# Performance work log

Measured on AMD Instinct MI355X. Metric: run time of the kernel, lower is better.

The kernel has to match this reference:

```python
import jax, jax.numpy as jnp
import numpy as np

TOPK = 16  # module init arg
EPS = 1e-12  # F.normalize eps


def setup_inputs() -> dict:
    key = jax.random.key(0)
    k1, k2, k3 = jax.random.split(key, 3)
    b, c, h, w = 2, 256, 96, 96
    rc = max(c // 4, 16)  # reduced_channels = 64
    x = jax.random.normal(k1, (b, c, h, w), dtype=jnp.float32)
    # 1x1 convs are channel-mixing matmuls; store weights as [out_ch, in_ch]
    w_reduce = jax.random.normal(k2, (rc, c), dtype=jnp.float32) * 0.05
    w_proj = jax.random.normal(k3, (c, rc), dtype=jnp.float32) * 0.05
    return {"x": x, "w_reduce": w_reduce, "w_proj": w_proj}


def reference(x, w_reduce, w_proj):
    b, c, h, w = x.shape
    n = h * w
    # reduce: 1x1 conv == channel matmul -> [b, rc, N]
    feat = jnp.einsum('rc,bchw->brhw', w_reduce, x).reshape(b, -1, n)
    # F.normalize(dim=1): divide by max(L2-norm over channels, eps)
    nrm = jnp.maximum(jnp.sqrt(jnp.sum(feat * feat, axis=1, keepdims=True)), EPS)
    nf = jnp.transpose(feat / nrm, (0, 2, 1))  # [b, N, rc]
    # cosine similarity matrix [b, N, N]
    sim = jnp.einsum('bnr,bmr->bnm', nf, nf)
    k = min(TOPK, n)
    _, idx = jax.lax.top_k(sim, k)  # [b, N, k]
    # gather top-k neighbor features and average -> [b, N, rc]
    corr = jax.vmap(lambda f, i: f[i].mean(axis=1))(nf, idx)
    # proj: 1x1 conv back to C channels, NCHW layout
    enhanced = jnp.einsum('cr,bnr->bnc', w_proj, corr)
    enhanced = jnp.transpose(enhanced, (0, 2, 1)).reshape(b, c, h, w)
    return x + enhanced
```

## Files before the change

### kernel.cpp

```cpp
#include <hip/hip_runtime.h>
#include <cstdint>
#include <cstddef>

#define NPIX 9216
#define NB 2
#define NC 256
#define RC 64
#define TK 16
#define NROWS (NB * NPIX)
#define CT 128
#define NQ 24
#define ECOLS 384
#define NTE 3
#define MAXC 128
#define LCAP 32
#define MARGIN 0.008f

typedef unsigned short ushort_t;
typedef unsigned int uint_t;
typedef __bf16 bf16x8 __attribute__((ext_vector_type(8)));
typedef float f32x4 __attribute__((ext_vector_type(4)));

__device__ __forceinline__ uint_t f2bf(float x) {
  uint_t u = __float_as_uint(x);
  return (u + 0x7FFFu + ((u >> 16) & 1u)) >> 16;
}

__device__ __forceinline__ uint_t ordu(float v) {
  uint_t u = __float_as_uint(v);
  return (u & 0x80000000u) ? ~u : (u | 0x80000000u);
}

#define GL2LDS(gsrc, ldst)                                                   \
  __builtin_amdgcn_global_load_lds(                                          \
      (const __attribute__((address_space(1))) uint_t*)(const void*)(gsrc),  \
      (__attribute__((address_space(3))) uint_t*)(void*)(ldst), 16, 0, 0)

__device__ __forceinline__ void stage_tile(
    const ushort_t* __restrict__ gtile, ushort_t* shbuf, int tid) {
  const int wave = tid >> 6, l = tid & 63;
  const int lr = l >> 3;
  const int ls = (l & 7) ^ lr;
  const ushort_t* g = gtile + (size_t)lr * 64 + ls * 8;
#pragma unroll
  for (int i = 0; i < 4; ++i) {
    const int j = wave * 4 + i;
    GL2LDS(g + (size_t)j * 512, shbuf + j * 512);
  }
}

__global__ __launch_bounds__(256) void k_reduce_norm(
    const float* __restrict__ x, const float* __restrict__ wr,
    float* __restrict__ nf, ushort_t* __restrict__ hi) {
  __shared__ float wl[NC * RC];
  const int tid = threadIdx.x;

  {
    float4 tmp[16];
    const float* wcol = wr + tid;
#pragma unroll
    for (int j = 0; j < 16; ++j) {
      tmp[j].x = wcol[(size_t)(4 * j + 0) * NC];
      tmp[j].y = wcol[(size_t)(4 * j + 1) * NC];
      tmp[j].z = wcol[(size_t)(4 * j + 2) * NC];
      tmp[j].w = wcol[(size_t)(4 * j + 3) * NC];
    }
    float4* wrow = (float4*)(wl + (size_t)tid * RC);
#pragma unroll
    for (int j = 0; j < 16; ++j) wrow[j] = tmp[j];
  }

  const int pl = tid >> 2, rq = tid & 3;
  const int row = blockIdx.x * 64 + pl;
  const int b = row >= NPIX;
  const int n = row - b * NPIX;
  const float* xp = x + (size_t)b * NC * NPIX + n;
  __syncthreads();

  float s[16];
#pragma unroll
  for (int i = 0; i < 16; ++i) s[i] = 0.f;

#pragma unroll 1
  for (int half = 0; half < 4; ++half) {
    float p4[16];
#pragma unroll
    for (int i = 0; i < 16; ++i) p4[i] = 0.f;
#pragma unroll 8
    for (int cl = 0; cl < 64; ++cl) {
      const int c = half * 64 + cl;
      const float xv = xp[(size_t)c * NPIX];
      const float4* w4 = (const float4*)(wl + c * RC + rq * 16);
#pragma unroll
      for (int i = 0; i < 4; ++i) {
        float4 w = w4[i];
        p4[i * 4 + 0] += w.x * xv; p4[i * 4 + 1] += w.y * xv;
        p4[i * 4 + 2] += w.z * xv; p4[i * 4 + 3] += w.w * xv;
      }
    }
#pragma unroll
    for (int i = 0; i < 16; ++i) s[i] += p4[i];
  }

  float ssq = 0.f;
#pragma unroll
  for (int i = 0; i < 4; ++i) {
    const float g = s[4 * i] * s[4 * i] + s[4 * i + 1] * s[4 * i + 1] +
                    s[4 * i + 2] * s[4 * i + 2] + s[4 * i + 3] * s[4 * i + 3];
    ssq += g;
  }
  ssq += __shfl_xor(ssq, 1);
  ssq += __shfl_xor(ssq, 2);
  const float inv = 1.f / fmaxf(sqrtf(ssq), 1e-12f);
#pragma unroll
  for (int i = 0; i < 16; ++i) s[i] *= inv;

  float4* no = (float4*)(nf + (size_t)row * RC + rq * 16);
#pragma unroll
  for (int i = 0; i < 4; ++i)
    no[i] = make_float4(s[i * 4], s[i * 4 + 1], s[i * 4 + 2], s[i * 4 + 3]);

  uint_t hs[16];
#pragma unroll
  for (int i = 0; i < 16; ++i) hs[i] = f2bf(s[i]);
  uint4* ho = (uint4*)(hi + (size_t)row * RC + rq * 16);
#pragma unroll
  for (int h = 0; h < 2; ++h)
    ho[h] = make_uint4(hs[h*8+0] | (hs[h*8+1] << 16), hs[h*8+2] | (hs[h*8+3] << 16),
                       hs[h*8+4] | (hs[h*8+5] << 16), hs[h*8+6] | (hs[h*8+7] << 16));
}

__global__ __launch_bounds__(256) void k_sim_max(
    const ushort_t* __restrict__ nf_hi, float* __restrict__ tmax) {
  __shared__ ushort_t sh[CT * 64];
  const int rb = blockIdx.x / NQ, q = blockIdx.x % NQ;
  const int tid = threadIdx.x, wave = tid >> 6, lane = tid & 63;
  const int n = lane & 15, quad = lane >> 4;
  const int r0 = rb * 128 + wave * 32 + n, r1 = r0 + 16;
  const int b = rb >= 72;
  const size_t cbase = (size_t)b * NPIX;
  const int x0 = (quad ^ (n & 7)) * 8;
  const int x1 = ((quad + 4) ^ (n & 7)) * 8;

  const bf16x8 bh00 = *(const bf16x8*)(nf_hi + (size_t)r0 * 64 + quad * 8);
  const bf16x8 bh01 = *(const bf16x8*)(nf_hi + (size_t)r0 * 64 + 32 + quad * 8);
  const bf16x8 bh10 = *(const bf16x8*)(nf_hi + (size_t)r1 * 64 + quad * 8);
  const bf16x8 bh11 = *(const bf16x8*)(nf_hi + (size_t)r1 * 64 + 32 + quad * 8);

  float cm0 = -1e30f, cm1 = -1e30f;
  const ushort_t* gtile = nf_hi + (cbase + q * ECOLS) * 64;

  for (int t = 0; t < NTE; ++t) {
    stage_tile(gtile, sh, tid);
    gtile += CT * 64;
    __syncthreads();

#pragma unroll
    for (int st = 0; st < 8; ++st) {
      const ushort_t* ap = sh + (st * 16 + n) * 64;
      bf16x8 ah0 = *(const bf16x8*)(ap + x0);
      bf16x8 ah1 = *(const bf16x8*)(ap + x1);
      f32x4 z = {0.f, 0.f, 0.f, 0.f};
      f32x4 a0 = __builtin_amdgcn_mfma_f32_16x16x32_bf16(ah0, bh00, z, 0, 0, 0);
      a0 = __builtin_amdgcn_mfma_f32_16x16x32_bf16(ah1, bh01, a0, 0, 0, 0);
      f32x4 a1 = __builtin_amdgcn_mfma_f32_16x16x32_bf16(ah0, bh10, z, 0, 0, 0);
      a1 = __builtin_amdgcn_mfma_f32_16x16x32_bf16(ah1, bh11, a1, 0, 0, 0);
      const float m0 = fmaxf(fmaxf(a0[0], a0[1]), fmaxf(a0[2], a0[3]));
      const float m1 = fmaxf(fmaxf(a1[0], a1[1]), fmaxf(a1[2], a1[3]));
      cm0 = fmaxf(cm0, m0);
      cm1 = fmaxf(cm1, m1);
    }
    __syncthreads();
  }
  tmax[(size_t)r0 * 96 + q * 4 + quad] = cm0;
  tmax[(size_t)r1 * 96 + q * 4 + quad] = cm1;
}

__global__ __launch_bounds__(256) void k_thresh(
    const float* __restrict__ tmax, float* __restrict__ Tb,
    int* __restrict__ rowcnt) {
  const int wave = threadIdx.x >> 6, lane = threadIdx.x & 63;
  const int row = blockIdx.x * 4 + wave;
  const float* tp = tmax + (size_t)row * 96;
  float v0 = tp[lane];
  float v1 = (lane < 32) ? tp[64 + lane] : -1e30f;
  float m = -1e30f;
#pragma unroll
  for (int k = 0; k < TK; ++k) {
    float c = fmaxf(v0, v1);
#pragma unroll
    for (int d = 1; d < 64; d <<= 1) c = fmaxf(c, __shfl_xor(c, d));
    m = c;
    if (v0 == m) v0 = -1e30f;
    if (v1 == m) v1 = -1e30f;
  }
  if (lane == 0) {
    Tb[row] = m - MARGIN;
    rowcnt[row] = 0;
  }
}

__global__ __launch_bounds__(256) void k_collect(
    const ushort_t* __restrict__ nf_hi, const float* __restrict__ Tb,
    int* __restrict__ cidx, int* __restrict__ rowcnt) {
  __shared__ ushort_t sh[CT * 64];
  __shared__ ushort_t lst[128][LCAP + 1];
  __shared__ int lcnt[128];
  const int rb = blockIdx.x / NQ, q = blockIdx.x % NQ;
  const int tid = threadIdx.x, wave = tid >> 6, lane = tid & 63;
  const int n = lane & 15, quad = lane >> 4;
  const int rl0 = wave * 32 + n, rl1 = rl0 + 16;
  const int r0 = rb * 128 + rl0, r1 = r0 + 16;
  const int b = rb >= 72;
  const size_t cbase = (size_t)b * NPIX;
  const int x0 = (quad ^ (n & 7)) * 8;
  const int x1 = ((quad + 4) ^ (n & 7)) * 8;

  if (tid < 128) lcnt[tid] = 0;

  const bf16x8 bh00 = *(const bf16x8*)(nf_hi + (size_t)r0 * 64 + quad * 8);
  const bf16x8 bh01 = *(const bf16x8*)(nf_hi + (size_t)r0 * 64 + 32 + quad * 8);
  const bf16x8 bh10 = *(const bf16x8*)(nf_hi + (size_t)r1 * 64 + quad * 8);
  const bf16x8 bh11 = *(const bf16x8*)(nf_hi + (size_t)r1 * 64 + 32 + quad * 8);

  const float T0 = Tb[r0], T1 = Tb[r1];
  const ushort_t* gtile = nf_hi + (cbase + q * ECOLS) * 64;

  for (int t = 0; t < NTE; ++t) {
    const int cb = q * ECOLS + t * CT;
    stage_tile(gtile, sh, tid);
    gtile += CT * 64;
    __syncthreads();

#pragma unroll
    for (int st = 0; st < 8; ++st) {
      const ushort_t* ap = sh + (st * 16 + n) * 64;
      bf16x8 ah0 = *(const bf16x8*)(ap + x0);
      bf16x8 ah1 = *(const bf16x8*)(ap + x1);
      f32x4 z = {0.f, 0.f, 0.f, 0.f};
      f32x4 a0 = __builtin_amdgcn_mfma_f32_16x16x32_bf16(ah0, bh00, z, 0, 0, 0);
      a0 = __builtin_amdgcn_mfma_f32_16x16x32_bf16(ah1, bh01, a0, 0, 0, 0);
      f32x4 a1 = __builtin_amdgcn_mfma_f32_16x16x32_bf16(ah0, bh10, z, 0, 0, 0);
      a1 = __builtin_amdgcn_mfma_f32_16x16x32_bf16(ah1, bh11, a1, 0, 0, 0);

      const int c0 = cb + st * 16 + quad * 4;
      const float mx0 = fmaxf(fmaxf(a0[0], a0[1]), fmaxf(a0[2], a0[3]));
      if (mx0 >= T0) {
        const int m0 = (a0[0] >= T0) | ((a0[1] >= T0) << 1) |
                       ((a0[2] >= T0) << 2) | ((a0[3] >= T0) << 3);
        int slot = atomicAdd(&lcnt[rl0], __popc(m0));
#pragma unroll
        for (int r = 0; r < 4; ++r)
          if (m0 & (1 << r)) {
            if (slot < LCAP) lst[rl0][slot] = (ushort_t)(c0 + r);
            ++slot;
          }
      }
      const float mx1 = fmaxf(fmaxf(a1[0], a1[1]), fmaxf(a1[2], a1[3]));
      if (mx1 >= T1) {
        const int m1 = (a1[0] >= T1) | ((a1[1] >= T1) << 1) |
                       ((a1[2] >= T1) << 2) | ((a1[3] >= T1) << 3);
        int slot = atomicAdd(&lcnt[rl1], __popc(m1));
#pragma unroll
        for (int r = 0; r < 4; ++r)
          if (m1 & (1 << r)) {
            if (slot < LCAP) lst[rl1][slot] = (ushort_t)(c0 + r);
            ++slot;
          }
      }
    }
    __syncthreads();
  }
  if (tid < 128) {
    const int row = rb * 128 + tid;
    const int cnt = min(lcnt[tid], LCAP);
    int base = atomicAdd(rowcnt + row, cnt);
    for (int j = 0; j < cnt; ++j) {
      const int gs = base + j;
      if (gs < MAXC) cidx[(size_t)row * MAXC + gs] = (int)lst[tid][j];
    }
  }
}

__global__ __launch_bounds__(256) void k_merge_gather(
    const float* __restrict__ nf, const int* __restrict__ cidx,
    const int* __restrict__ rowcnt, float* __restrict__ corr) {
  __shared__ ushort_t selc[4][TK];
  const int wave = threadIdx.x >> 6, lane = threadIdx.x & 63;
  const int row = blockIdx.x * 4 + wave;
  const int b = row >= NPIX;
  const int rl = row - b * NPIX;
  const float* nfb = nf + (size_t)b * NPIX * RC;

  const int cv = cidx[(size_t)row * MAXC + lane];
  const int C = min(rowcnt[row], MAXC);

  if (lane < TK) selc[wave][lane] = (ushort_t)rl;

  float4 rv[16];
  const float4* r4 = (const float4*)(nf + (size_t)row * RC);
#pragma unroll
  for (int i = 0; i < 16; ++i) rv[i] = r4[i];

  unsigned long long k0 = 0;
  int c0;
  {
    c0 = (lane < C) ? cv : rl;
    const float4* g = (const float4*)(nfb + (size_t)c0 * RC);
    float s = 0.f;
#pragma unroll
    for (int i = 0; i < 16; ++i) {
      float4 a = g[i];
      s += a.x * rv[i].x + a.y * rv[i].y + a.z * rv[i].z + a.w * rv[i].w;
    }
    if (lane < C)
      k0 = ((unsigned long long)ordu(s) << 32) | (uint_t)(~(uint_t)c0);
  }

  if (C <= 64) {
    unsigned long long thr = 0;
#pragma unroll
    for (int bit = 63; bit >= 0; --bit) {
      const unsigned long long cand = thr | (1ull << bit);
      if (__popcll(__ballot(k0 >= cand)) >= TK) thr = cand;
    }
    if (thr != 0) {
      const unsigned long long ml = (lane == 0) ? 0ull : (~0ull >> (64 - lane));
      const unsigned long long b0 = __ballot(k0 >= thr);
      if (k0 >= thr) {
        const int r = __popcll(b0 & ml);
        if (r < TK) selc[wave][r] = (ushort_t)c0;
      }
    }
  } else {
    unsigned long long k1 = 0;
    int c1;
    {
      c1 = (64 + lane < C) ? cidx[(size_t)row * MAXC + 64 + lane] : rl;
      const float4* g = (const float4*)(nfb + (size_t)c1 * RC);
      float s = 0.f;
#pragma unroll
      for (int i = 0; i < 16; ++i) {
        float4 a = g[i];
        s += a.x * rv[i].x + a.y * rv[i].y + a.z * rv[i].z + a.w * rv[i].w;
      }
      if (64 + lane < C)
        k1 = ((unsigned long long)ordu(s) << 32) | (uint_t)(~(uint_t)c1);
    }
    unsigned long long thr = 0;
#pragma unroll
    for (int bit = 63; bit >= 0; --bit) {
      const unsigned long long cand = thr | (1ull << bit);
      const int cnt = __popcll(__ballot(k0 >= cand)) + __popcll(__ballot(k1 >= cand));
      if (cnt >= TK) thr = cand;
    }
    if (thr != 0) {
      const unsigned long long ml = (lane == 0) ? 0ull : (~0ull >> (64 - lane));
      const unsigned long long b0 = __ballot(k0 >= thr);
      const unsigned long long b1 = __ballot(k1 >= thr);
      const int n0 = __popcll(b0);
      if (k0 >= thr) {
        const int r = __popcll(b0 & ml);
        if (r < TK) selc[wave][r] = (ushort_t)c0;
      }
      if (k1 >= thr) {
        const int r = n0 + __popcll(b1 & ml);
        if (r < TK) selc[wave][r] = (ushort_t)c1;
      }
    }
  }

  asm volatile("" ::: "memory");

  float acc = 0.f;
#pragma unroll
  for (int t = 0; t < TK; ++t)
    acc += nfb[(size_t)selc[wave][t] * RC + lane];
  corr[(size_t)row * RC + lane] = acc * 0.0625f;
}

__global__ __launch_bounds__(128) void k_proj_add(
    const float* __restrict__ x, const float* __restrict__ wp,
    const float* __restrict__ corr, float* __restrict__ out) {
  const int pg = blockIdx.x >> 3, cq = blockIdx.x & 7;
  const int tid = threadIdx.x;

  __shared__ float wl[32 * RC];
  {
    const float4* src = (const float4*)(wp + (size_t)cq * 32 * RC);
    float4* dst = (float4*)wl;
#pragma unroll
    for (int i = 0; i < 4; ++i) dst[i * 128 + tid] = src[i * 128 + tid];
  }

  const int p = pg * 128 + tid;
  const int b = p >= NPIX;
  const int n = p - b * NPIX;

  float4 cr[16];
  const float4* c4 = (const float4*)(corr + (size_t)p * RC);
#pragma unroll
  for (int i = 0; i < 16; ++i) cr[i] = c4[i];
  __syncthreads();

  const size_t xb = (size_t)b * NC * NPIX + n;
  for (int cl = 0; cl < 32; ++cl) {
    const float4* w4 = (const float4*)(wl + cl * RC);
    float s = 0.f;
#pragma unroll
    for (int i = 0; i < 16; ++i) {
      float4 w = w4[i];
      s += w.x * cr[i].x + w.y * cr[i].y + w.z * cr[i].z + w.w * cr[i].w;
    }
    const int c = cq * 32 + cl;
    const size_t oi = xb + (size_t)c * NPIX;
    out[oi] = x[oi] + s;
  }
}

extern "C" void kernel_launch(void* const* d_in, const int* in_sizes, int n_in,
                              void* d_out, int out_size, void* d_ws, size_t ws_size,
                              hipStream_t stream) {
  const float* x = (const float*)d_in[0];
  const float* wr = (const float*)d_in[1];
  const float* wp = (const float*)d_in[2];
  float* out = (float*)d_out;

  char* ws = (char*)d_ws;
  float* tmax = (float*)ws;
  float* corr = (float*)ws;
  float* nf = (float*)(ws + 18874368);
  ushort_t* nf_hi = (ushort_t*)(ws + 23592960);
  float* Tb = (float*)(ws + 25952256);
  int* rowcnt = (int*)(ws + 26025984);
  int* cidx = (int*)(ws + 26099712);

  hipLaunchKernelGGL(k_reduce_norm, dim3(288), dim3(256), 0, stream, x, wr, nf, nf_hi);
  hipLaunchKernelGGL(k_sim_max, dim3(144 * NQ), dim3(256), 0, stream, nf_hi, tmax);
  hipLaunchKernelGGL(k_thresh, dim3(NROWS / 4), dim3(256), 0, stream, tmax, Tb, rowcnt);
  hipLaunchKernelGGL(k_collect, dim3(144 * NQ), dim3(256), 0, stream,
                     nf_hi, Tb, cidx, rowcnt);
  hipLaunchKernelGGL(k_merge_gather, dim3(NROWS / 4), dim3(256), 0, stream,
                     nf, cidx, rowcnt, corr);
  hipLaunchKernelGGL(k_proj_add, dim3(1152), dim3(128), 0, stream, x, wp, corr, out);
}
```

Measured before the change: 255.4 us.

## Restructure reduce-norm kernel to split channels across lanes and drop LDS weights

The reduce+normalize kernel now assigns 16 threads per pixel, each covering one quarter of the input channels and 16 output channels. Partial sums are combined with shuffles, and the grid grows from 288 to 1152 blocks. The 64KB shared-memory weight staging is removed and weights are read directly from global/L2 as float4. This raises occupancy and parallelism for the first stage. In exchange it adds shuffle reduction work, more register pressure from 64 cached x values, and weight reads that each thread repeats through the cache.

```diff
diff --git a/kernel.cpp b/kernel.cpp
--- a/kernel.cpp
+++ b/kernel.cpp
@@ -52,54 +52,43 @@
 __global__ __launch_bounds__(256) void k_reduce_norm(
     const float* __restrict__ x, const float* __restrict__ wr,
     float* __restrict__ nf, ushort_t* __restrict__ hi) {
-  __shared__ float wl[NC * RC];
   const int tid = threadIdx.x;
-
-  {
-    float4 tmp[16];
-    const float* wcol = wr + tid;
-#pragma unroll
-    for (int j = 0; j < 16; ++j) {
-      tmp[j].x = wcol[(size_t)(4 * j + 0) * NC];
-      tmp[j].y = wcol[(size_t)(4 * j + 1) * NC];
-      tmp[j].z = wcol[(size_t)(4 * j + 2) * NC];
-      tmp[j].w = wcol[(size_t)(4 * j + 3) * NC];
-    }
-    float4* wrow = (float4*)(wl + (size_t)tid * RC);
-#pragma unroll
-    for (int j = 0; j < 16; ++j) wrow[j] = tmp[j];
-  }
-
-  const int pl = tid >> 2, rq = tid & 3;
-  const int row = blockIdx.x * 64 + pl;
+  const int px = tid >> 4, rq = (tid >> 2) & 3, cq = tid & 3;
+  const int lane = tid & 63;
+  const int row = blockIdx.x * 16 + px;
   const int b = row >= NPIX;
   const int n = row - b * NPIX;
-  const float* xp = x + (size_t)b * NC * NPIX + n;
-  __syncthreads();
+  const float* xp = x + (size_t)b * NC * NPIX + (size_t)cq * 64 * NPIX + n;
+
+  float xv[64];
+#pragma unroll
+  for (int j = 0; j < 64; ++j) xv[j] = xp[(size_t)j * NPIX];
 
   float s[16];
-#pragma unroll
-  for (int i = 0; i < 16; ++i) s[i] = 0.f;
-
-#pragma unroll 1
-  for (int half = 0; half < 4; ++half) {
-    float p4[16];
-#pragma unroll
-    for (int i = 0; i < 16; ++i) p4[i] = 0.f;
-#pragma unroll 8
-    for (int cl = 0; cl < 64; ++cl) {
-      const int c = half * 64 + cl;
-      const float xv = xp[(size_t)c * NPIX];
-      const float4* w4 = (const float4*)(wl + c * RC + rq * 16);
-#pragma unroll
-      for (int i = 0; i < 4; ++i) {
-        float4 w = w4[i];
-        p4[i * 4 + 0] += w.x * xv; p4[i * 4 + 1] += w.y * xv;
-        p4[i * 4 + 2] += w.z * xv; p4[i * 4 + 3] += w.w * xv;
-      }
-    }
-#pragma unroll
-    for (int i = 0; i < 16; ++i) s[i] += p4[i];
+  const float* wbase = wr + (size_t)(rq * 16) * NC + cq * 64;
+#pragma unroll
+  for (int i = 0; i < 16; ++i) {
+    const float4* w4 = (const float4*)(wbase + (size_t)i * NC);
+    float acc = 0.f;
+#pragma unroll
+    for (int j4 = 0; j4 < 16; ++j4) {
+      float4 w = w4[j4];
+      acc += w.x * xv[4 * j4 + 0];
+      acc += w.y * xv[4 * j4 + 1];
+      acc += w.z * xv[4 * j4 + 2];
+      acc += w.w * xv[4 * j4 + 3];
+    }
+    s[i] = acc;
+  }
+
+  const int gbase = lane & ~3;
+#pragma unroll
+  for (int i = 0; i < 16; ++i) {
+    const float p0 = __shfl(s[i], gbase + 0);
+    const float p1 = __shfl(s[i], gbase + 1);
+    const float p2 = __shfl(s[i], gbase + 2);
+    const float p3 = __shfl(s[i], gbase + 3);
+    s[i] = ((p0 + p1) + p2) + p3;
   }
 
   float ssq = 0.f;
@@ -109,25 +98,23 @@
                     s[4 * i + 2] * s[4 * i + 2] + s[4 * i + 3] * s[4 * i + 3];
     ssq += g;
   }
-  ssq += __shfl_xor(ssq, 1);
-  ssq += __shfl_xor(ssq, 2);
+  ssq += __shfl_xor(ssq, 4);
+  ssq += __shfl_xor(ssq, 8);
   const float inv = 1.f / fmaxf(sqrtf(ssq), 1e-12f);
 #pragma unroll
   for (int i = 0; i < 16; ++i) s[i] *= inv;
 
-  float4* no = (float4*)(nf + (size_t)row * RC + rq * 16);
-#pragma unroll
-  for (int i = 0; i < 4; ++i)
-    no[i] = make_float4(s[i * 4], s[i * 4 + 1], s[i * 4 + 2], s[i * 4 + 3]);
-
-  uint_t hs[16];
-#pragma unroll
-  for (int i = 0; i < 16; ++i) hs[i] = f2bf(s[i]);
-  uint4* ho = (uint4*)(hi + (size_t)row * RC + rq * 16);
-#pragma unroll
-  for (int h = 0; h < 2; ++h)
-    ho[h] = make_uint4(hs[h*8+0] | (hs[h*8+1] << 16), hs[h*8+2] | (hs[h*8+3] << 16),
-                       hs[h*8+4] | (hs[h*8+5] << 16), hs[h*8+6] | (hs[h*8+7] << 16));
+  *(float4*)(nf + (size_t)row * RC + rq * 16 + cq * 4) =
+      make_float4(s[4 * cq + 0], s[4 * cq + 1], s[4 * cq + 2], s[4 * cq + 3]);
+
+  if (cq < 2) {
+    uint_t hs[8];
+#pragma unroll
+    for (int k = 0; k < 8; ++k) hs[k] = f2bf(s[cq * 8 + k]);
+    *(uint4*)(hi + (size_t)row * RC + rq * 16 + cq * 8) =
+        make_uint4(hs[0] | (hs[1] << 16), hs[2] | (hs[3] << 16),
+                   hs[4] | (hs[5] << 16), hs[6] | (hs[7] << 16));
+  }
 }
 
 __global__ __launch_bounds__(256) void k_sim_max(
@@ -435,7 +422,7 @@
   int* rowcnt = (int*)(ws + 26025984);
   int* cidx = (int*)(ws + 26099712);
 
-  hipLaunchKernelGGL(k_reduce_norm, dim3(288), dim3(256), 0, stream, x, wr, nf, nf_hi);
+  hipLaunchKernelGGL(k_reduce_norm, dim3(1152), dim3(256), 0, stream, x, wr, nf, nf_hi);
   hipLaunchKernelGGL(k_sim_max, dim3(144 * NQ), dim3(256), 0, stream, nf_hi, tmax);
   hipLaunchKernelGGL(k_thresh, dim3(NROWS / 4), dim3(256), 0, stream, tmax, Tb, rowcnt);
   hipLaunchKernelGGL(k_collect, dim3(144 * NQ), dim3(256), 0, stream,
```

After: 371.2 us. 45.3% more time.
